# Kernel optimization log

Measured on AMD Instinct MI355X. Metric: run time of the kernel, lower is better.

Reference implementation:

```python
import jax, jax.numpy as jnp
import numpy as np

B, C, H, W = 16, 256, 64, 64
HEADS = 8


def setup_inputs() -> dict:
    key = jax.random.key(0)
    ks = jax.random.split(key, 12)
    s = 0.02
    return {
        "x": jax.random.normal(ks[0], (B, C, H, W), jnp.float32),
        "Wq": jax.random.normal(ks[1], (C, C), jnp.float32) * s,
        "bq": jnp.zeros((C,), jnp.float32),
        "Wk": jax.random.normal(ks[2], (C, C), jnp.float32) * s,
        "bk": jnp.zeros((C,), jnp.float32),
        "Wv": jax.random.normal(ks[3], (C, C), jnp.float32) * s,
        "bv": jnp.zeros((C,), jnp.float32),
        "gamma": jax.random.normal(ks[4], (1,), jnp.float32) * 0.5,
        "beta": jax.random.normal(ks[5], (1,), jnp.float32) * 0.5,
        "W1": jax.random.normal(ks[6], (C, C), jnp.float32) * s,
        "b1": jnp.zeros((C,), jnp.float32),
        "u1": jax.random.normal(ks[7], (C,), jnp.float32),
        "W2": jax.random.normal(ks[8], (C, C), jnp.float32) * s,
        "b2": jnp.zeros((C,), jnp.float32),
        "u2": jax.random.normal(ks[9], (C,), jnp.float32),
    }


def _conv1x1(x, Wt, b):
    # 1x1 conv == per-pixel GEMM over channels
    return jnp.einsum('oc,bchw->bohw', Wt, x) + b[None, :, None, None]


def _l2(v):
    return v / (jnp.linalg.norm(v) + 1e-12)


def _spectral_norm(Wt, u):
    # one power iteration (torch SpectralNorm wrapper), u treated as buffer
    Wm = Wt.reshape(Wt.shape[0], -1)
    v = _l2(Wm.T @ u)
    u_new = _l2(Wm @ v)
    sigma = u_new @ (Wm @ v)
    return Wt / sigma


def reference(x, Wq, bq, Wk, bk, Wv, bv, gamma, beta, W1, b1, u1, W2, b2, u2):
    Bn, Cn, Hh, Ww = x.shape
    N = Hh * Ww
    d = Cn // HEADS
    scale = HEADS ** (-0.5)
    # 1x1 conv projections, then b (h n) s layout -> (B, heads, d, N)
    q = _conv1x1(x, Wq, bq).reshape(Bn, HEADS, d, N)
    k = _conv1x1(x, Wk, bk).reshape(Bn, HEADS, d, N)
    v = _conv1x1(x, Wv, bv).reshape(Bn, HEADS, d, N)
    # per-head channel attention: energy is (B, heads, d, d)
    energy = jnp.einsum('bhis,bhjs->bhij', q, k) * scale
    attn = jax.nn.softmax(energy, axis=-1)
    out = jnp.einsum('bhij,bhjs->bhis', attn, v).reshape(Bn, Cn, Hh, Ww)
    out = gamma * out + x
    # residual refinement net (dropout = identity in eval mode)
    y = _conv1x1(out, _spectral_norm(W1, u1), b1)
    y = jax.nn.leaky_relu(y, 0.1)
    y = _conv1x1(y, _spectral_norm(W2, u2), b2)
    out = out + beta * y
    return (out, attn)
```

## Files before the change

### kernel.cpp

```cpp
#include <hip/hip_runtime.h>
#include <hip/hip_bf16.h>
#include <cstdint>
#include <cstddef>

typedef __attribute__((ext_vector_type(8))) __bf16 bf16x8;
typedef __attribute__((ext_vector_type(4))) float f32x4;
typedef __attribute__((ext_vector_type(8))) unsigned short us8;
typedef __attribute__((ext_vector_type(4))) unsigned short us4;

__device__ __forceinline__ unsigned short f2bf(float f){
  unsigned int u = __float_as_uint(f);
  u += 0x7fffu + ((u >> 16) & 1u);
  return (unsigned short)(u >> 16);
}
__device__ __forceinline__ float bf2f(unsigned short h){
  return __uint_as_float(((unsigned int)h) << 16);
}
__device__ __forceinline__ bf16x8 ldbf8(const unsigned short* p){
  return __builtin_bit_cast(bf16x8, *(const us8*)p);
}
__device__ __forceinline__ void split16(const float* __restrict__ g,
                                        unsigned short* __restrict__ hs,
                                        unsigned short* __restrict__ ls){
  #pragma unroll
  for (int q = 0; q < 4; ++q){
    float4 v = *(const float4*)(g + q*4);
    unsigned short h0=f2bf(v.x), h1=f2bf(v.y), h2=f2bf(v.z), h3=f2bf(v.w);
    us4 hv = {h0,h1,h2,h3};
    us4 lv = { f2bf(v.x - bf2f(h0)), f2bf(v.y - bf2f(h1)),
               f2bf(v.z - bf2f(h2)), f2bf(v.w - bf2f(h3)) };
    *(us4*)(hs + q*4) = hv;
    *(us4*)(ls + q*4) = lv;
  }
}

#define SCALE_E 0.35355339059327373f

static const size_t OFF_XHI    = 0;
static const size_t OFF_XLO    = 33554432;
static const size_t OFF_XTHI   = 67108864;
static const size_t OFF_GPART  = 100663296;
static const size_t OFF_G      = 113246208;
static const size_t OFF_M      = 117440512;
static const size_t OFF_W1S    = 119537664;
static const size_t OFF_W2S    = 119668736;
static const size_t OFF_SIG    = 119799808;
static const size_t OFF_XSUM   = 119799824;
static const size_t OFF_ROWADD = 119816208;

__global__ void k_zero(float* __restrict__ xsum){
  xsum[blockIdx.x * 256 + threadIdx.x] = 0.f;
}

__global__ void k_sigma(const float* __restrict__ W1, const float* __restrict__ u1,
                        const float* __restrict__ W2, const float* __restrict__ u2,
                        float* __restrict__ sig){
  const float* W = blockIdx.x ? W2 : W1;
  const float* u = blockIdx.x ? u2 : u1;
  int t = threadIdx.x;
  __shared__ __align__(16) float red[256];
  __shared__ __align__(16) float vls[256];
  __shared__ __align__(16) float uls[256];
  uls[t] = u[t];
  __syncthreads();
  float t1 = 0.f;
  for (int o = 0; o < 256; ++o) t1 += W[o*256 + t] * uls[o];
  red[t] = t1 * t1;
  __syncthreads();
  for (int s = 128; s > 0; s >>= 1){ if (t < s) red[t] += red[t+s]; __syncthreads(); }
  float nrm = sqrtf(red[0]);
  vls[t] = t1 / (nrm + 1e-12f);
  __syncthreads();
  float w = 0.f;
  const float4* wr4 = (const float4*)(W + t*256);
  for (int c4 = 0; c4 < 64; ++c4){
    float4 a = wr4[c4];
    float4 v = *(const float4*)&vls[c4*4];
    w += a.x*v.x + a.y*v.y + a.z*v.z + a.w*v.w;
  }
  __syncthreads();
  red[t] = w * w;
  __syncthreads();
  for (int s = 128; s > 0; s >>= 1){ if (t < s) red[t] += red[t+s]; __syncthreads(); }
  if (t == 0){
    float s2 = red[0];
    float sn = sqrtf(s2);
    sig[blockIdx.x] = s2 / (sn + 1e-12f);
  }
}

__global__ void k_wconv(const float* __restrict__ W1, const float* __restrict__ W2,
                        const float* __restrict__ sig,
                        unsigned short* __restrict__ W1s, unsigned short* __restrict__ W2s){
  int sel = blockIdx.x >> 6;
  const float* W = sel ? W2 : W1;
  unsigned short* o = sel ? W2s : W1s;
  float inv = 1.0f / sig[sel];
  int base = (blockIdx.x & 63) * 1024 + threadIdx.x * 4;
  float4 v = *(const float4*)&W[base];
  us4 r = { f2bf(v.x*inv), f2bf(v.y*inv), f2bf(v.z*inv), f2bf(v.w*inv) };
  *(us4*)&o[base] = r;
}

__global__ __launch_bounds__(256) void k_convert(const float* __restrict__ x,
    unsigned short* __restrict__ xhi, unsigned short* __restrict__ xlo,
    unsigned short* __restrict__ xthi, float* __restrict__ xsum){
  int b = blockIdx.z, c0 = blockIdx.y*64, n0 = blockIdx.x*64;
  int t = threadIdx.x, tn = t & 15, tc = t >> 4;
  __shared__ __align__(16) unsigned short hs[64][68];
  __shared__ __align__(16) float ps[64][17];
  #pragma unroll
  for (int rr = 0; rr < 4; ++rr){
    int cl = rr*16 + tc;
    size_t gro = ((size_t)(b*256 + c0 + cl))*4096 + n0 + tn*4;
    float4 v = *(const float4*)&x[gro];
    unsigned short h0=f2bf(v.x), h1=f2bf(v.y), h2=f2bf(v.z), h3=f2bf(v.w);
    us4 hv = {h0,h1,h2,h3};
    us4 lv = { f2bf(v.x - bf2f(h0)), f2bf(v.y - bf2f(h1)),
               f2bf(v.z - bf2f(h2)), f2bf(v.w - bf2f(h3)) };
    *(us4*)&xhi[gro] = hv;
    *(us4*)&xlo[gro] = lv;
    *(us4*)&hs[cl][tn*4] = hv;
    ps[cl][tn] = v.x + v.y + v.z + v.w;
  }
  __syncthreads();
  #pragma unroll
  for (int rr = 0; rr < 4; ++rr){
    int nl = rr*16 + tc;
    int cl4 = tn*4;
    us4 w = { hs[cl4+0][nl], hs[cl4+1][nl], hs[cl4+2][nl], hs[cl4+3][nl] };
    *(us4*)&xthi[((size_t)(b*4096 + n0 + nl))*256 + c0 + cl4] = w;
  }
  if (t < 64){
    float s = 0.f;
    #pragma unroll
    for (int k = 0; k < 16; ++k) s += ps[t][k];
    atomicAdd(&xsum[b*256 + c0 + t], s);
  }
}

__global__ __launch_bounds__(256) void k_gram(const unsigned short* __restrict__ xhi,
    const unsigned short* __restrict__ xlo, float* __restrict__ G, float* __restrict__ Gp){
  int b = blockIdx.z;
  int tr = (blockIdx.y >> 1) * 128, tc = (blockIdx.y & 1) * 128;
  int kc = blockIdx.x * 1024;
  int t = threadIdx.x;
  __shared__ __align__(16) unsigned short Ah[128*40], Al[128*40], Bh[128*40], Bl[128*40];
  f32x4 acc[4][4];
  #pragma unroll
  for (int i = 0; i < 4; ++i)
    #pragma unroll
    for (int j = 0; j < 4; ++j) acc[i][j] = (f32x4){0.f,0.f,0.f,0.f};
  int srow = t >> 1, skh = (t & 1) * 16;
  int l = t & 63, wv = t >> 6;
  int wr = (wv >> 1) * 64, wc = (wv & 1) * 64;
  int lr = l & 15, lg = l >> 4;
  size_t bb = (size_t)b * 256 * 4096;
  for (int kk = kc; kk < kc + 1024; kk += 32){
    __syncthreads();
    size_t ga = bb + (size_t)(tr + srow)*4096 + kk + skh;
    size_t gb = bb + (size_t)(tc + srow)*4096 + kk + skh;
    *(us8*)&Ah[srow*40 + skh]     = *(const us8*)&xhi[ga];
    *(us8*)&Ah[srow*40 + skh + 8] = *(const us8*)&xhi[ga + 8];
    *(us8*)&Al[srow*40 + skh]     = *(const us8*)&xlo[ga];
    *(us8*)&Al[srow*40 + skh + 8] = *(const us8*)&xlo[ga + 8];
    *(us8*)&Bh[srow*40 + skh]     = *(const us8*)&xhi[gb];
    *(us8*)&Bh[srow*40 + skh + 8] = *(const us8*)&xhi[gb + 8];
    *(us8*)&Bl[srow*40 + skh]     = *(const us8*)&xlo[gb];
    *(us8*)&Bl[srow*40 + skh + 8] = *(const us8*)&xlo[gb + 8];
    __syncthreads();
    bf16x8 ah[4], alv[4], bh[4], blv[4];
    #pragma unroll
    for (int i = 0; i < 4; ++i){
      ah[i]  = ldbf8(&Ah[(wr + i*16 + lr)*40 + lg*8]);
      alv[i] = ldbf8(&Al[(wr + i*16 + lr)*40 + lg*8]);
      bh[i]  = ldbf8(&Bh[(wc + i*16 + lr)*40 + lg*8]);
      blv[i] = ldbf8(&Bl[(wc + i*16 + lr)*40 + lg*8]);
    }
    #pragma unroll
    for (int i = 0; i < 4; ++i)
      #pragma unroll
      for (int j = 0; j < 4; ++j){
        acc[i][j] = __builtin_amdgcn_mfma_f32_16x16x32_bf16(ah[i],  bh[j],  acc[i][j], 0,0,0);
        acc[i][j] = __builtin_amdgcn_mfma_f32_16x16x32_bf16(ah[i],  blv[j], acc[i][j], 0,0,0);
        acc[i][j] = __builtin_amdgcn_mfma_f32_16x16x32_bf16(alv[i], bh[j],  acc[i][j], 0,0,0);
      }
  }
  float* dst = (blockIdx.x == 0) ? (G + (size_t)b*65536)
                                 : (Gp + ((size_t)(blockIdx.x - 1)*16 + b)*65536);
  #pragma unroll
  for (int i = 0; i < 4; ++i)
    #pragma unroll
    for (int j = 0; j < 4; ++j)
      #pragma unroll
      for (int r = 0; r < 4; ++r){
        int row = tr + wr + i*16 + lg*4 + r;
        int col = tc + wc + j*16 + lr;
        dst[row*256 + col] = acc[i][j][r];
      }
}

__global__ void k_gred(const float* __restrict__ G0, const float* __restrict__ Gp,
                       unsigned short* __restrict__ Ghi, unsigned short* __restrict__ Glo){
  size_t idx = ((size_t)blockIdx.x * 256 + threadIdx.x) * 4;
  float4 g  = *(const float4*)&G0[idx];
  float4 p0 = *(const float4*)&Gp[idx];
  float4 p1 = *(const float4*)&Gp[idx + 1048576];
  float4 p2 = *(const float4*)&Gp[idx + 2097152];
  float s0 = g.x + p0.x + p1.x + p2.x;
  float s1 = g.y + p0.y + p1.y + p2.y;
  float s2 = g.z + p0.z + p1.z + p2.z;
  float s3 = g.w + p0.w + p1.w + p2.w;
  unsigned short h0=f2bf(s0), h1=f2bf(s1), h2=f2bf(s2), h3=f2bf(s3);
  us4 hv = {h0,h1,h2,h3};
  us4 lv = { f2bf(s0 - bf2f(h0)), f2bf(s1 - bf2f(h1)),
             f2bf(s2 - bf2f(h2)), f2bf(s3 - bf2f(h3)) };
  *(us4*)&Ghi[idx] = hv;
  *(us4*)&Glo[idx] = lv;
}

__global__ __launch_bounds__(256) void k_qg(const float* __restrict__ Wq,
    const unsigned short* __restrict__ Ghi, const unsigned short* __restrict__ Glo,
    unsigned short* __restrict__ Phi, unsigned short* __restrict__ Plo){
  int b = blockIdx.z;
  int tr = blockIdx.y * 128, tc = blockIdx.x * 128;
  int t = threadIdx.x;
  __shared__ __align__(16) unsigned short Ah[128*40], Al[128*40], Bh[128*40], Bl[128*40];
  f32x4 acc[4][4];
  #pragma unroll
  for (int i = 0; i < 4; ++i)
    #pragma unroll
    for (int j = 0; j < 4; ++j) acc[i][j] = (f32x4){0.f,0.f,0.f,0.f};
  int srow = t >> 1, skh = (t & 1) * 16;
  int l = t & 63, wv = t >> 6;
  int wr = (wv >> 1) * 64, wc = (wv & 1) * 64;
  int lr = l & 15, lg = l >> 4;
  for (int kk = 0; kk < 256; kk += 32){
    __syncthreads();
    split16(Wq + (size_t)(tr + srow)*256 + kk + skh, &Ah[srow*40 + skh], &Al[srow*40 + skh]);
    size_t gb = (size_t)b*65536 + (size_t)(tc + srow)*256 + kk + skh;
    *(us8*)&Bh[srow*40 + skh]     = *(const us8*)&Ghi[gb];
    *(us8*)&Bh[srow*40 + skh + 8] = *(const us8*)&Ghi[gb + 8];
    *(us8*)&Bl[srow*40 + skh]     = *(const us8*)&Glo[gb];
    *(us8*)&Bl[srow*40 + skh + 8] = *(const us8*)&Glo[gb + 8];
    __syncthreads();
    bf16x8 ah[4], alv[4], bh[4], blv[4];
    #pragma unroll
    for (int i = 0; i < 4; ++i){
      ah[i]  = ldbf8(&Ah[(wr + i*16 + lr)*40 + lg*8]);
      alv[i] = ldbf8(&Al[(wr + i*16 + lr)*40 + lg*8]);
      bh[i]  = ldbf8(&Bh[(wc + i*16 + lr)*40 + lg*8]);
      blv[i] = ldbf8(&Bl[(wc + i*16 + lr)*40 + lg*8]);
    }
    #pragma unroll
    for (int i = 0; i < 4; ++i)
      #pragma unroll
      for (int j = 0; j < 4; ++j){
        acc[i][j] = __builtin_amdgcn_mfma_f32_16x16x32_bf16(ah[i],  bh[j],  acc[i][j], 0,0,0);
        acc[i][j] = __builtin_amdgcn_mfma_f32_16x16x32_bf16(ah[i],  blv[j], acc[i][j], 0,0,0);
        acc[i][j] = __builtin_amdgcn_mfma_f32_16x16x32_bf16(alv[i], bh[j],  acc[i][j], 0,0,0);
      }
  }
  #pragma unroll
  for (int i = 0; i < 4; ++i)
    #pragma unroll
    for (int j = 0; j < 4; ++j)
      #pragma unroll
      for (int r = 0; r < 4; ++r){
        int row = tr + wr + i*16 + lg*4 + r;
        int col = tc + wc + j*16 + lr;
        size_t off = (size_t)b*65536 + (size_t)row*256 + col;
        float p = acc[i][j][r];
        unsigned short hp = f2bf(p);
        Phi[off] = hp;
        Plo[off] = f2bf(p - bf2f(hp));
      }
}

__global__ __launch_bounds__(256) void k_e(const unsigned short* __restrict__ Phi,
    const unsigned short* __restrict__ Plo, const float* __restrict__ Wk,
    float* __restrict__ Ef){
  int b = blockIdx.z;
  int tr = blockIdx.y * 128, tc = blockIdx.x * 128;
  int t = threadIdx.x;
  __shared__ __align__(16) unsigned short Ah[128*40], Al[128*40], Bh[128*40], Bl[128*40];
  f32x4 acc[4][4];
  #pragma unroll
  for (int i = 0; i < 4; ++i)
    #pragma unroll
    for (int j = 0; j < 4; ++j) acc[i][j] = (f32x4){0.f,0.f,0.f,0.f};
  int srow = t >> 1, skh = (t & 1) * 16;
  int l = t & 63, wv = t >> 6;
  int wr = (wv >> 1) * 64, wc = (wv & 1) * 64;
  int lr = l & 15, lg = l >> 4;
  for (int kk = 0; kk < 256; kk += 32){
    __syncthreads();
    size_t ga = (size_t)b*65536 + (size_t)(tr + srow)*256 + kk + skh;
    *(us8*)&Ah[srow*40 + skh]     = *(const us8*)&Phi[ga];
    *(us8*)&Ah[srow*40 + skh + 8] = *(const us8*)&Phi[ga + 8];
    *(us8*)&Al[srow*40 + skh]     = *(const us8*)&Plo[ga];
    *(us8*)&Al[srow*40 + skh + 8] = *(const us8*)&Plo[ga + 8];
    split16(Wk + (size_t)(tc + srow)*256 + kk + skh, &Bh[srow*40 + skh], &Bl[srow*40 + skh]);
    __syncthreads();
    bf16x8 ah[4], alv[4], bh[4], blv[4];
    #pragma unroll
    for (int i = 0; i < 4; ++i){
      ah[i]  = ldbf8(&Ah[(wr + i*16 + lr)*40 + lg*8]);
      alv[i] = ldbf8(&Al[(wr + i*16 + lr)*40 + lg*8]);
      bh[i]  = ldbf8(&Bh[(wc + i*16 + lr)*40 + lg*8]);
      blv[i] = ldbf8(&Bl[(wc + i*16 + lr)*40 + lg*8]);
    }
    #pragma unroll
    for (int i = 0; i < 4; ++i)
      #pragma unroll
      for (int j = 0; j < 4; ++j){
        acc[i][j] = __builtin_amdgcn_mfma_f32_16x16x32_bf16(ah[i],  bh[j],  acc[i][j], 0,0,0);
        acc[i][j] = __builtin_amdgcn_mfma_f32_16x16x32_bf16(ah[i],  blv[j], acc[i][j], 0,0,0);
        acc[i][j] = __builtin_amdgcn_mfma_f32_16x16x32_bf16(alv[i], bh[j],  acc[i][j], 0,0,0);
      }
  }
  #pragma unroll
  for (int i = 0; i < 4; ++i)
    #pragma unroll
    for (int j = 0; j < 4; ++j)
      #pragma unroll
      for (int r = 0; r < 4; ++r){
        int row = tr + wr + i*16 + lg*4 + r;
        int col = tc + wc + j*16 + lr;
        Ef[(size_t)b*65536 + (size_t)row*256 + col] = SCALE_E * acc[i][j][r];
      }
}

__global__ __launch_bounds__(256) void k_soft(const float* __restrict__ Ef,
    const float* __restrict__ Wq, const float* __restrict__ bq,
    const float* __restrict__ Wk, const float* __restrict__ bk,
    const float* __restrict__ Wv, const float* __restrict__ bv,
    const float* __restrict__ gptr, const float* __restrict__ xsum,
    unsigned short* __restrict__ Mw, float* __restrict__ rowadd,
    float* __restrict__ attn_out){
  int blk = blockIdx.x, b = blk >> 3, h = blk & 7;
  int t = threadIdx.x;
  int i = t >> 3, j4 = (t & 7) * 4;
  __shared__ __align__(16) float Aw[32][40];
  __shared__ float qsv[32], ksv[32];
  if (t < 64){
    int r = t & 31;
    const float* Wm = (t < 32) ? Wq : Wk;
    const float4* wr4 = (const float4*)(Wm + (size_t)(h*32 + r)*256);
    const float4* xs4 = (const float4*)(xsum + b*256);
    float s = 0.f;
    #pragma unroll
    for (int c4 = 0; c4 < 64; ++c4){
      float4 a = wr4[c4], xv = xs4[c4];
      s += a.x*xv.x + a.y*xv.y + a.z*xv.z + a.w*xv.w;
    }
    if (t < 32) qsv[r] = s; else ksv[r] = s;
  }
  __syncthreads();
  float4 e = *(const float4*)&Ef[(size_t)b*65536 + (size_t)(h*32 + i)*256 + h*32 + j4];
  float bqi = bq[h*32 + i];
  float qb  = qsv[i] + 4096.f * bqi;
  e.x += SCALE_E * (bqi*ksv[j4+0] + bk[h*32+j4+0]*qb);
  e.y += SCALE_E * (bqi*ksv[j4+1] + bk[h*32+j4+1]*qb);
  e.z += SCALE_E * (bqi*ksv[j4+2] + bk[h*32+j4+2]*qb);
  e.w += SCALE_E * (bqi*ksv[j4+3] + bk[h*32+j4+3]*qb);
  float m = fmaxf(fmaxf(e.x, e.y), fmaxf(e.z, e.w));
  m = fmaxf(m, __shfl_xor(m, 1));
  m = fmaxf(m, __shfl_xor(m, 2));
  m = fmaxf(m, __shfl_xor(m, 4));
  float ex0 = expf(e.x - m), ex1 = expf(e.y - m), ex2 = expf(e.z - m), ex3 = expf(e.w - m);
  float s = ex0 + ex1 + ex2 + ex3;
  s += __shfl_xor(s, 1); s += __shfl_xor(s, 2); s += __shfl_xor(s, 4);
  float inv = 1.f / s;
  float4 a4 = { ex0*inv, ex1*inv, ex2*inv, ex3*inv };
  *(float4*)&attn_out[(((size_t)(b*8 + h))*32 + i)*32 + j4] = a4;
  *(float4*)&Aw[i][j4] = a4;
  __syncthreads();
  float gamma = gptr[0];
  float mr[32];
  #pragma unroll
  for (int r = 0; r < 32; ++r) mr[r] = 0.f;
  for (int j = 0; j < 32; ++j){
    float wvv = Wv[(size_t)(h*32 + j)*256 + t];
    #pragma unroll
    for (int r = 0; r < 32; ++r) mr[r] += Aw[r][j] * wvv;
  }
  unsigned short* Mrow = Mw + ((size_t)b*256 + h*32)*256 + t;
  #pragma unroll
  for (int r = 0; r < 32; ++r) Mrow[r*256] = f2bf(gamma * mr[r]);
  if (t < 32){
    float sr = 0.f;
    #pragma unroll
    for (int j = 0; j < 32; ++j) sr += Aw[t][j] * bv[h*32 + j];
    rowadd[b*256 + h*32 + t] = gamma * sr;
  }
}

template<int MODE>
__global__ __launch_bounds__(256) void k_gemm(const unsigned short* __restrict__ Aall,
    const unsigned short* __restrict__ Bmat, const unsigned short* __restrict__ xthi,
    const float* __restrict__ rowadd, const float* __restrict__ bias,
    const float* __restrict__ betap, float* __restrict__ osc,
    unsigned short* __restrict__ outb){
  int b = blockIdx.z;
  int n0 = blockIdx.x * 128, o0 = blockIdx.y * 128;
  int t = threadIdx.x;
  __shared__ __align__(16) unsigned short Als[128*40], Bls[128*40];
  f32x4 acc[4][4];
  #pragma unroll
  for (int i = 0; i < 4; ++i)
    #pragma unroll
    for (int j = 0; j < 4; ++j) acc[i][j] = (f32x4){0.f,0.f,0.f,0.f};
  const unsigned short* A  = Aall + (size_t)b * 1048576;
  const unsigned short* Bp = (MODE == 0) ? (Bmat + (size_t)b * 65536) : Bmat;
  int srow = t >> 1, skh = (t & 1) * 16;
  int l = t & 63, wv = t >> 6;
  int wr = (wv >> 1) * 64, wc = (wv & 1) * 64;
  int lr = l & 15, lg = l >> 4;
  for (int kk = 0; kk < 256; kk += 32){
    __syncthreads();
    const unsigned short* ga = A  + (size_t)(n0 + srow)*256 + kk + skh;
    const unsigned short* gb = Bp + (size_t)(o0 + srow)*256 + kk + skh;
    *(us8*)&Als[srow*40 + skh]     = *(const us8*)ga;
    *(us8*)&Als[srow*40 + skh + 8] = *(const us8*)(ga + 8);
    *(us8*)&Bls[srow*40 + skh]     = *(const us8*)gb;
    *(us8*)&Bls[srow*40 + skh + 8] = *(const us8*)(gb + 8);
    __syncthreads();
    bf16x8 af[4], bfv[4];
    #pragma unroll
    for (int i = 0; i < 4; ++i) af[i]  = ldbf8(&Als[(wr + i*16 + lr)*40 + lg*8]);
    #pragma unroll
    for (int j = 0; j < 4; ++j) bfv[j] = ldbf8(&Bls[(wc + j*16 + lr)*40 + lg*8]);
    #pragma unroll
    for (int i = 0; i < 4; ++i)
      #pragma unroll
      for (int j = 0; j < 4; ++j)
        acc[i][j] = __builtin_amdgcn_mfma_f32_16x16x32_bf16(af[i], bfv[j], acc[i][j], 0,0,0);
  }
  float beta = (MODE == 2) ? betap[0] : 0.f;
  #pragma unroll
  for (int j = 0; j < 4; ++j){
    int oc = o0 + wc + j*16 + lr;
    float bvl = (MODE == 0) ? rowadd[b*256 + oc] : bias[oc];
    #pragma unroll
    for (int i = 0; i < 4; ++i){
      #pragma unroll
      for (int r = 0; r < 4; ++r){
        int n = n0 + wr + i*16 + lg*4 + r;
        size_t off = ((size_t)b*4096 + n)*256 + oc;
        float v = acc[i][j][r];
        if (MODE == 0){
          v += bf2f(xthi[off]) + bvl;
          osc[off] = v;
          outb[off] = f2bf(v);
        } else if (MODE == 1){
          v += bvl;
          v = (v > 0.f) ? v : 0.1f * v;
          outb[off] = f2bf(v);
        } else {
          v = osc[off] + beta * (v + bvl);
          outb[off] = f2bf(v);
        }
      }
    }
  }
}

__global__ __launch_bounds__(256) void k_tpose(const unsigned short* __restrict__ fin,
                                               float* __restrict__ out){
  int b = blockIdx.z, c0 = blockIdx.y*64, n0 = blockIdx.x*64;
  int t = threadIdx.x, tn = t & 15, tc = t >> 4;
  __shared__ __align__(16) unsigned short ts[64][68];
  #pragma unroll
  for (int rr = 0; rr < 4; ++rr){
    int nl = rr*16 + tc;
    us4 v = *(const us4*)&fin[((size_t)(b*4096 + n0 + nl))*256 + c0 + tn*4];
    *(us4*)&ts[nl][tn*4] = v;
  }
  __syncthreads();
  #pragma unroll
  for (int rr = 0; rr < 4; ++rr){
    int cl = rr*16 + tc;
    int nl4 = tn*4;
    float4 v = { bf2f(ts[nl4+0][cl]), bf2f(ts[nl4+1][cl]),
                 bf2f(ts[nl4+2][cl]), bf2f(ts[nl4+3][cl]) };
    *(float4*)&out[((size_t)(b*256 + c0 + cl))*4096 + n0 + nl4] = v;
  }
}

extern "C" void kernel_launch(void* const* d_in, const int* in_sizes, int n_in,
                              void* d_out, int out_size, void* d_ws, size_t ws_size,
                              hipStream_t stream){
  const float* x    = (const float*)d_in[0];
  const float* Wq   = (const float*)d_in[1];
  const float* bq   = (const float*)d_in[2];
  const float* Wk   = (const float*)d_in[3];
  const float* bk   = (const float*)d_in[4];
  const float* Wv   = (const float*)d_in[5];
  const float* bv   = (const float*)d_in[6];
  const float* gamma= (const float*)d_in[7];
  const float* beta = (const float*)d_in[8];
  const float* W1   = (const float*)d_in[9];
  const float* b1   = (const float*)d_in[10];
  const float* u1   = (const float*)d_in[11];
  const float* W2   = (const float*)d_in[12];
  const float* b2   = (const float*)d_in[13];
  const float* u2   = (const float*)d_in[14];

  char* ws = (char*)d_ws;
  unsigned short* xhi   = (unsigned short*)(ws + OFF_XHI);
  unsigned short* xlo   = (unsigned short*)(ws + OFF_XLO);
  unsigned short* xthi  = (unsigned short*)(ws + OFF_XTHI);
  float*          Gp    = (float*)(ws + OFF_GPART);
  float*          G0    = (float*)(ws + OFF_G);
  unsigned short* Mw    = (unsigned short*)(ws + OFF_M);
  unsigned short* W1s   = (unsigned short*)(ws + OFF_W1S);
  unsigned short* W2s   = (unsigned short*)(ws + OFF_W2S);
  float*          sig   = (float*)(ws + OFF_SIG);
  float*          xsum  = (float*)(ws + OFF_XSUM);
  float*          rowadd= (float*)(ws + OFF_ROWADD);
  unsigned short* Ghi   = (unsigned short*)(ws + OFF_XLO);
  unsigned short* Glo   = (unsigned short*)(ws + OFF_XLO + 2097152);
  unsigned short* Phi   = (unsigned short*)(ws + OFF_GPART);
  unsigned short* Plo   = (unsigned short*)(ws + OFF_GPART + 2097152);
  float*          Ef    = (float*)(ws + OFF_GPART + 4194304);
  unsigned short* othi  = xlo;
  unsigned short* y1t   = xhi;
  unsigned short* finT  = xthi;

  float* outF  = (float*)d_out;
  float* attnO = outF + 16777216;
  float* osc   = outF;

  k_zero<<<dim3(16), dim3(256), 0, stream>>>(xsum);
  k_sigma<<<dim3(2), dim3(256), 0, stream>>>(W1, u1, W2, u2, sig);
  k_wconv<<<dim3(128), dim3(256), 0, stream>>>(W1, W2, sig, W1s, W2s);
  k_convert<<<dim3(64,4,16), dim3(256), 0, stream>>>(x, xhi, xlo, xthi, xsum);
  k_gram<<<dim3(4,4,16), dim3(256), 0, stream>>>(xhi, xlo, G0, Gp);
  k_gred<<<dim3(1024), dim3(256), 0, stream>>>(G0, Gp, Ghi, Glo);
  k_qg<<<dim3(2,2,16), dim3(256), 0, stream>>>(Wq, Ghi, Glo, Phi, Plo);
  k_e<<<dim3(2,2,16), dim3(256), 0, stream>>>(Phi, Plo, Wk, Ef);
  k_soft<<<dim3(128), dim3(256), 0, stream>>>(Ef, Wq, bq, Wk, bk, Wv, bv,
                                              gamma, xsum, Mw, rowadd, attnO);
  k_gemm<0><<<dim3(32,2,16), dim3(256), 0, stream>>>(xthi, Mw, xthi, rowadd, b1, beta, osc, othi);
  k_gemm<1><<<dim3(32,2,16), dim3(256), 0, stream>>>(othi, W1s, xthi, rowadd, b1, beta, osc, y1t);
  k_gemm<2><<<dim3(32,2,16), dim3(256), 0, stream>>>(y1t, W2s, xthi, rowadd, b2, beta, osc, finT);
  k_tpose<<<dim3(64,4,16), dim3(256), 0, stream>>>(finT, outF);
}
```

Baseline: 424.5 us.

## Double-buffer LDS with register prefetch in gram/gemm; fold residual into M

The gram and projection GEMM kernels now prefetch the next K tile into registers while computing on the current tile, using double-buffered shared memory so only one barrier per iteration is needed. The residual x is folded into the mixing matrix M as an identity diagonal, which removes the xthi read in the first GEMM epilogue. The fp32 intermediate 'osc' write/read is dropped, and the final GEMM reads the bf16 intermediate instead. This cuts memory traffic and barrier stalls, at the cost of more LDS and registers, and the residual path now carries bf16 rounding of out.

```diff
diff --git a/kernel.cpp b/kernel.cpp
--- a/kernel.cpp
+++ b/kernel.cpp
@@ -145,7 +145,8 @@
   int tr = (blockIdx.y >> 1) * 128, tc = (blockIdx.y & 1) * 128;
   int kc = blockIdx.x * 1024;
   int t = threadIdx.x;
-  __shared__ __align__(16) unsigned short Ah[128*40], Al[128*40], Bh[128*40], Bl[128*40];
+  __shared__ __align__(16) unsigned short Ah[2][128*40], Al[2][128*40],
+                                          Bh[2][128*40], Bl[2][128*40];
   f32x4 acc[4][4];
   #pragma unroll
   for (int i = 0; i < 4; ++i)
@@ -156,26 +157,39 @@
   int wr = (wv >> 1) * 64, wc = (wv & 1) * 64;
   int lr = l & 15, lg = l >> 4;
   size_t bb = (size_t)b * 256 * 4096;
-  for (int kk = kc; kk < kc + 1024; kk += 32){
-    __syncthreads();
-    size_t ga = bb + (size_t)(tr + srow)*4096 + kk + skh;
-    size_t gb = bb + (size_t)(tc + srow)*4096 + kk + skh;
-    *(us8*)&Ah[srow*40 + skh]     = *(const us8*)&xhi[ga];
-    *(us8*)&Ah[srow*40 + skh + 8] = *(const us8*)&xhi[ga + 8];
-    *(us8*)&Al[srow*40 + skh]     = *(const us8*)&xlo[ga];
-    *(us8*)&Al[srow*40 + skh + 8] = *(const us8*)&xlo[ga + 8];
-    *(us8*)&Bh[srow*40 + skh]     = *(const us8*)&xhi[gb];
-    *(us8*)&Bh[srow*40 + skh + 8] = *(const us8*)&xhi[gb + 8];
-    *(us8*)&Bl[srow*40 + skh]     = *(const us8*)&xlo[gb];
-    *(us8*)&Bl[srow*40 + skh + 8] = *(const us8*)&xlo[gb + 8];
+  const unsigned short* gah = xhi + bb + (size_t)(tr + srow)*4096 + kc + skh;
+  const unsigned short* gal = xlo + bb + (size_t)(tr + srow)*4096 + kc + skh;
+  const unsigned short* gbh = xhi + bb + (size_t)(tc + srow)*4096 + kc + skh;
+  const unsigned short* gbl = xlo + bb + (size_t)(tc + srow)*4096 + kc + skh;
+  us8 rah0 = *(const us8*)gah, rah1 = *(const us8*)(gah + 8);
+  us8 ral0 = *(const us8*)gal, ral1 = *(const us8*)(gal + 8);
+  us8 rbh0 = *(const us8*)gbh, rbh1 = *(const us8*)(gbh + 8);
+  us8 rbl0 = *(const us8*)gbl, rbl1 = *(const us8*)(gbl + 8);
+  int cur = 0;
+  for (int ki = 0; ki < 32; ++ki){
+    *(us8*)&Ah[cur][srow*40 + skh]     = rah0;
+    *(us8*)&Ah[cur][srow*40 + skh + 8] = rah1;
+    *(us8*)&Al[cur][srow*40 + skh]     = ral0;
+    *(us8*)&Al[cur][srow*40 + skh + 8] = ral1;
+    *(us8*)&Bh[cur][srow*40 + skh]     = rbh0;
+    *(us8*)&Bh[cur][srow*40 + skh + 8] = rbh1;
+    *(us8*)&Bl[cur][srow*40 + skh]     = rbl0;
+    *(us8*)&Bl[cur][srow*40 + skh + 8] = rbl1;
+    if (ki < 31){
+      int ko = (ki + 1) * 32;
+      rah0 = *(const us8*)(gah + ko); rah1 = *(const us8*)(gah + ko + 8);
+      ral0 = *(const us8*)(gal + ko); ral1 = *(const us8*)(gal + ko + 8);
+      rbh0 = *(const us8*)(gbh + ko); rbh1 = *(const us8*)(gbh + ko + 8);
+      rbl0 = *(const us8*)(gbl + ko); rbl1 = *(const us8*)(gbl + ko + 8);
+    }
     __syncthreads();
     bf16x8 ah[4], alv[4], bh[4], blv[4];
     #pragma unroll
     for (int i = 0; i < 4; ++i){
-      ah[i]  = ldbf8(&Ah[(wr + i*16 + lr)*40 + lg*8]);
-      alv[i] = ldbf8(&Al[(wr + i*16 + lr)*40 + lg*8]);
-      bh[i]  = ldbf8(&Bh[(wc + i*16 + lr)*40 + lg*8]);
-      blv[i] = ldbf8(&Bl[(wc + i*16 + lr)*40 + lg*8]);
+      ah[i]  = ldbf8(&Ah[cur][(wr + i*16 + lr)*40 + lg*8]);
+      alv[i] = ldbf8(&Al[cur][(wr + i*16 + lr)*40 + lg*8]);
+      bh[i]  = ldbf8(&Bh[cur][(wc + i*16 + lr)*40 + lg*8]);
+      blv[i] = ldbf8(&Bl[cur][(wc + i*16 + lr)*40 + lg*8]);
     }
     #pragma unroll
     for (int i = 0; i < 4; ++i)
@@ -185,6 +199,7 @@
         acc[i][j] = __builtin_amdgcn_mfma_f32_16x16x32_bf16(ah[i],  blv[j], acc[i][j], 0,0,0);
         acc[i][j] = __builtin_amdgcn_mfma_f32_16x16x32_bf16(alv[i], bh[j],  acc[i][j], 0,0,0);
       }
+    cur ^= 1;
   }
   float* dst = (blockIdx.x == 0) ? (G + (size_t)b*65536)
                                  : (Gp + ((size_t)(blockIdx.x - 1)*16 + b)*65536);
@@ -387,7 +402,10 @@
   }
   unsigned short* Mrow = Mw + ((size_t)b*256 + h*32)*256 + t;
   #pragma unroll
-  for (int r = 0; r < 32; ++r) Mrow[r*256] = f2bf(gamma * mr[r]);
+  for (int r = 0; r < 32; ++r){
+    float diag = (h*32 + r == t) ? 1.f : 0.f;
+    Mrow[r*256] = f2bf(gamma * mr[r] + diag);
+  }
   if (t < 32){
     float sr = 0.f;
     #pragma unroll
@@ -398,14 +416,14 @@
 
 template<int MODE>
 __global__ __launch_bounds__(256) void k_gemm(const unsigned short* __restrict__ Aall,
-    const unsigned short* __restrict__ Bmat, const unsigned short* __restrict__ xthi,
+    const unsigned short* __restrict__ Bmat, const unsigned short* __restrict__ oth,
     const float* __restrict__ rowadd, const float* __restrict__ bias,
-    const float* __restrict__ betap, float* __restrict__ osc,
+    const float* __restrict__ betap,
     unsigned short* __restrict__ outb){
   int b = blockIdx.z;
   int n0 = blockIdx.x * 128, o0 = blockIdx.y * 128;
   int t = threadIdx.x;
-  __shared__ __align__(16) unsigned short Als[128*40], Bls[128*40];
+  __shared__ __align__(16) unsigned short Als[2][128*40], Bls[2][128*40];
   f32x4 acc[4][4];
   #pragma unroll
   for (int i = 0; i < 4; ++i)
@@ -417,20 +435,28 @@
   int l = t & 63, wv = t >> 6;
   int wr = (wv >> 1) * 64, wc = (wv & 1) * 64;
   int lr = l & 15, lg = l >> 4;
-  for (int kk = 0; kk < 256; kk += 32){
-    __syncthreads();
-    const unsigned short* ga = A  + (size_t)(n0 + srow)*256 + kk + skh;
-    const unsigned short* gb = Bp + (size_t)(o0 + srow)*256 + kk + skh;
-    *(us8*)&Als[srow*40 + skh]     = *(const us8*)ga;
-    *(us8*)&Als[srow*40 + skh + 8] = *(const us8*)(ga + 8);
-    *(us8*)&Bls[srow*40 + skh]     = *(const us8*)gb;
-    *(us8*)&Bls[srow*40 + skh + 8] = *(const us8*)(gb + 8);
+  const unsigned short* ga = A  + (size_t)(n0 + srow)*256 + skh;
+  const unsigned short* gb = Bp + (size_t)(o0 + srow)*256 + skh;
+  us8 ra0 = *(const us8*)ga, ra1 = *(const us8*)(ga + 8);
+  us8 rb0 = *(const us8*)gb, rb1 = *(const us8*)(gb + 8);
+  #pragma unroll
+  for (int ki = 0; ki < 8; ++ki){
+    int cur = ki & 1;
+    *(us8*)&Als[cur][srow*40 + skh]     = ra0;
+    *(us8*)&Als[cur][srow*40 + skh + 8] = ra1;
+    *(us8*)&Bls[cur][srow*40 + skh]     = rb0;
+    *(us8*)&Bls[cur][srow*40 + skh + 8] = rb1;
+    if (ki < 7){
+      int ko = (ki + 1) * 32;
+      ra0 = *(const us8*)(ga + ko); ra1 = *(const us8*)(ga + ko + 8);
+      rb0 = *(const us8*)(gb + ko); rb1 = *(const us8*)(gb + ko + 8);
+    }
     __syncthreads();
     bf16x8 af[4], bfv[4];
     #pragma unroll
-    for (int i = 0; i < 4; ++i) af[i]  = ldbf8(&Als[(wr + i*16 + lr)*40 + lg*8]);
-    #pragma unroll
-    for (int j = 0; j < 4; ++j) bfv[j] = ldbf8(&Bls[(wc + j*16 + lr)*40 + lg*8]);
+    for (int i = 0; i < 4; ++i) af[i]  = ldbf8(&Als[cur][(wr + i*16 + lr)*40 + lg*8]);
+    #pragma unroll
+    for (int j = 0; j < 4; ++j) bfv[j] = ldbf8(&Bls[cur][(wc + j*16 + lr)*40 + lg*8]);
     #pragma unroll
     for (int i = 0; i < 4; ++i)
       #pragma unroll
@@ -450,15 +476,14 @@
         size_t off = ((size_t)b*4096 + n)*256 + oc;
         float v = acc[i][j][r];
         if (MODE == 0){
-          v += bf2f(xthi[off]) + bvl;
-          osc[off] = v;
+          v += bvl;
           outb[off] = f2bf(v);
         } else if (MODE == 1){
           v += bvl;
           v = (v > 0.f) ? v : 0.1f * v;
           outb[off] = f2bf(v);
         } else {
-          v = osc[off] + beta * (v + bvl);
+          v = bf2f(oth[off]) + beta * (v + bvl);
           outb[off] = f2bf(v);
         }
       }
@@ -530,7 +555,6 @@
 
   float* outF  = (float*)d_out;
   float* attnO = outF + 16777216;
-  float* osc   = outF;
 
   k_zero<<<dim3(16), dim3(256), 0, stream>>>(xsum);
   k_sigma<<<dim3(2), dim3(256), 0, stream>>>(W1, u1, W2, u2, sig);
@@ -542,8 +566,8 @@
   k_e<<<dim3(2,2,16), dim3(256), 0, stream>>>(Phi, Plo, Wk, Ef);
   k_soft<<<dim3(128), dim3(256), 0, stream>>>(Ef, Wq, bq, Wk, bk, Wv, bv,
                                               gamma, xsum, Mw, rowadd, attnO);
-  k_gemm<0><<<dim3(32,2,16), dim3(256), 0, stream>>>(xthi, Mw, xthi, rowadd, b1, beta, osc, othi);
-  k_gemm<1><<<dim3(32,2,16), dim3(256), 0, stream>>>(othi, W1s, xthi, rowadd, b1, beta, osc, y1t);
-  k_gemm<2><<<dim3(32,2,16), dim3(256), 0, stream>>>(y1t, W2s, xthi, rowadd, b2, beta, osc, finT);
+  k_gemm<0><<<dim3(32,2,16), dim3(256), 0, stream>>>(xthi, Mw, othi, rowadd, b1, beta, othi);
+  k_gemm<1><<<dim3(32,2,16), dim3(256), 0, stream>>>(othi, W1s, othi, rowadd, b1, beta, y1t);
+  k_gemm<2><<<dim3(32,2,16), dim3(256), 0, stream>>>(y1t, W2s, othi, rowadd, b2, beta, finT);
   k_tpose<<<dim3(64,4,16), dim3(256), 0, stream>>>(finT, outF);
 }
```

Result: faster. 371.8 us (-12.4%).
